# Kernel optimization log

Hardware: AMD Instinct MI355X
Metric: run time of the kernel (lower is better)

Reference implementation:

```python
import jax, jax.numpy as jnp
import numpy as np

DIM = 256
WINDOW = 512  # look_backward=1, look_forward=0, causal


def setup_inputs() -> dict:
    key = jax.random.key(0)
    ks = jax.random.split(key, 7)
    B, N, D = 8, 8192, DIM
    s = D ** -0.5
    return {
        "x": jax.random.normal(ks[0], (B, D, N), dtype=jnp.float32),
        "Wq": jax.random.normal(ks[1], (D, D), dtype=jnp.float32) * s,
        "bq": jax.random.normal(ks[2], (D,), dtype=jnp.float32) * 0.01,
        "Wk": jax.random.normal(ks[3], (D, D), dtype=jnp.float32) * s,
        "bk": jax.random.normal(ks[4], (D,), dtype=jnp.float32) * 0.01,
        "Wv": jax.random.normal(ks[5], (D, D), dtype=jnp.float32) * s,
        "bv": jax.random.normal(ks[6], (D,), dtype=jnp.float32) * 0.01,
    }


def _local_attention(q, k, v, window):
    # q,k,v: (B, N, D); causal sliding-window attention, look_backward=1 window.
    b, n, d = q.shape
    nw = n // window  # N assumed multiple of window (autopad no-op here)
    scale = d ** -0.5
    qb = q.reshape(b, nw, window, d)
    kb = k.reshape(b, nw, window, d)
    vb = v.reshape(b, nw, window, d)

    def look_back(t):
        prev = jnp.pad(t, ((0, 0), (1, 0), (0, 0), (0, 0)))[:, :-1]
        return jnp.concatenate([prev, t], axis=2)  # (b, nw, 2*window, d)

    kb2 = look_back(kb)
    vb2 = look_back(vb)

    pos = jnp.arange(n).reshape(nw, window)
    prev_pos = jnp.pad(pos, ((1, 0), (0, 0)), constant_values=-1)[:-1]
    kpos = jnp.concatenate([prev_pos, pos], axis=1)  # (nw, 2*window)
    # causal mask + mask out the (nonexistent) window before window 0
    mask = (pos[:, :, None] >= kpos[:, None, :]) & (kpos[:, None, :] >= 0)

    scores = jnp.einsum('bnqd,bnkd->bnqk', qb, kb2) * scale
    scores = jnp.where(mask[None], scores, jnp.asarray(-1e9, scores.dtype))
    attn = jax.nn.softmax(scores, axis=-1)  # dropout(0.1) omitted: eval mode
    out = jnp.einsum('bnqk,bnkd->bnqd', attn, vb2)
    return out.reshape(b, n, d)


def reference(x, Wq, bq, Wk, bk, Wv, bv):
    # x: (B, D, N) -> permute -> (B, N, D)
    xp = jnp.transpose(x, (0, 2, 1))
    q = xp @ Wq.T + bq
    k = xp @ Wk.T + bk
    v = xp @ Wv.T + bv
    y = xp + _local_attention(q, k, v, WINDOW)  # residual
    return jnp.transpose(y, (0, 2, 1))
```

## Files before the change

kernel.cpp:

```cpp
#include <hip/hip_runtime.h>
#include <hip/hip_bf16.h>

#define DIM  256
#define NSEQ 8192
#define BATCH 8
#define WIN  512

typedef __attribute__((ext_vector_type(8))) short short8;
typedef __attribute__((ext_vector_type(4))) float floatx4;

union PFU { int i[4]; short8 v; };

__device__ __forceinline__ int packbf(float a, float b) {
    __hip_bfloat162 h;
    h.x = __float2bfloat16(a);
    h.y = __float2bfloat16(b);
    int r;
    __builtin_memcpy(&r, &h, 4);
    return r;
}

__global__ __launch_bounds__(256) void k_wcast(const float* __restrict__ w0,
                                               const float* __restrict__ w1,
                                               const float* __restrict__ w2,
                                               __hip_bfloat16* __restrict__ wb) {
    int i = (blockIdx.x * 256 + threadIdx.x) * 4;
    const float* s = (i < 65536) ? (w0 + i) : ((i < 131072) ? (w1 + i - 65536) : (w2 + i - 131072));
    float4 v = *(const float4*)s;
    union { __hip_bfloat16 h[4]; ushort4 u; } cv;
    cv.h[0] = __float2bfloat16(v.x);
    cv.h[1] = __float2bfloat16(v.y);
    cv.h[2] = __float2bfloat16(v.z);
    cv.h[3] = __float2bfloat16(v.w);
    *(ushort4*)(wb + i) = cv.u;
}

__global__ __launch_bounds__(256, 3) void k_prep(const float* __restrict__ x,
                                                 const __hip_bfloat16* __restrict__ wb,
                                                 const float* __restrict__ bq,
                                                 const float* __restrict__ bk,
                                                 const float* __restrict__ bv,
                                                 __hip_bfloat16* __restrict__ qo,
                                                 __hip_bfloat16* __restrict__ ko,
                                                 __hip_bfloat16* __restrict__ vto) {
    __shared__ float ftile[64][68];
    __shared__ __align__(16) char As[32768];
    const int b   = blockIdx.y;
    const int n0  = blockIdx.x * 64;
    const int tid = threadIdx.x;
    const int wv  = tid >> 6;
    const int l   = tid & 63;
    const int lm  = l & 15;
    const int qd  = l >> 4;
    const int wn  = wv * 64;

    const float* xb = x + (size_t)b * DIM * NSEQ;

    const int dr = l >> 4, nseg = l & 15;
#pragma unroll
    for (int dsl = 0; dsl < 4; ++dsl) {
        const int d0 = dsl * 64;
#pragma unroll
        for (int i = 0; i < 4; ++i) {
            const int r = wv * 16 + i * 4 + dr;
            float4 v = *(const float4*)(xb + (size_t)(d0 + r) * NSEQ + n0 + nseg * 4);
            *(float4*)&ftile[r][nseg * 4] = v;
        }
        __syncthreads();
#pragma unroll
        for (int p = 0; p < 2; ++p) {
            const int ks = dsl * 2 + p;
            int4 pk;
            int* pki = (int*)&pk;
#pragma unroll
            for (int jj = 0; jj < 4; ++jj)
                pki[jj] = packbf(ftile[p * 32 + wv * 8 + jj * 2][l],
                                 ftile[p * 32 + wv * 8 + jj * 2 + 1][l]);
            *(int4*)(As + ks * 4096 + wv * 1024 + l * 16) = pk;
        }
        __syncthreads();
    }

#pragma unroll
    for (int mode = 0; mode < 3; ++mode) {
        const __hip_bfloat16* wp = wb + mode * 65536;
        floatx4 acc[4][4];
#pragma unroll
        for (int i = 0; i < 4; ++i)
#pragma unroll
            for (int j = 0; j < 4; ++j) acc[i][j] = (floatx4){0.f, 0.f, 0.f, 0.f};

#pragma unroll
        for (int ks = 0; ks < 8; ++ks) {
            short8 wf[4], af[4];
#pragma unroll
            for (int j = 0; j < 4; ++j)
                wf[j] = *(const short8*)(wp + (size_t)(wn + j * 16 + lm) * DIM + ks * 32 + qd * 8);
#pragma unroll
            for (int j = 0; j < 4; ++j)
                af[j] = *(const short8*)(As + ks * 4096 + qd * 1024 + (j * 16 + lm) * 16);
            if (mode < 2) {
#pragma unroll
                for (int mt = 0; mt < 4; ++mt)
#pragma unroll
                    for (int nt = 0; nt < 4; ++nt)
                        acc[mt][nt] = __builtin_amdgcn_mfma_f32_16x16x32_bf16(af[mt], wf[nt], acc[mt][nt], 0, 0, 0);
            } else {
#pragma unroll
                for (int jw = 0; jw < 4; ++jw)
#pragma unroll
                    for (int ja = 0; ja < 4; ++ja)
                        acc[jw][ja] = __builtin_amdgcn_mfma_f32_16x16x32_bf16(wf[jw], af[ja], acc[jw][ja], 0, 0, 0);
            }
        }

        if (mode < 2) {
            const float* bias = mode ? bk : bq;
            __hip_bfloat16* op = (mode ? ko : qo) + (size_t)b * NSEQ * DIM;
            float bc[4];
#pragma unroll
            for (int nt = 0; nt < 4; ++nt) bc[nt] = bias[wn + nt * 16 + lm];
#pragma unroll
            for (int mt = 0; mt < 4; ++mt)
#pragma unroll
                for (int nt = 0; nt < 4; ++nt)
#pragma unroll
                    for (int r = 0; r < 4; ++r)
                        op[(size_t)(n0 + mt * 16 + qd * 4 + r) * DIM + wn + nt * 16 + lm] =
                            __float2bfloat16(acc[mt][nt][r] + bc[nt]);
        } else {
            __hip_bfloat16* op = vto + (size_t)b * DIM * NSEQ;
#pragma unroll
            for (int jw = 0; jw < 4; ++jw)
#pragma unroll
                for (int r = 0; r < 4; ++r) {
                    const int d = wn + jw * 16 + qd * 4 + r;
                    const float bb = bv[d];
#pragma unroll
                    for (int ja = 0; ja < 4; ++ja)
                        op[(size_t)d * NSEQ + n0 + ja * 16 + lm] =
                            __float2bfloat16(acc[jw][ja][r] + bb);
                }
        }
    }
}

__global__ __launch_bounds__(512, 2) void k_attn(const __hip_bfloat16* __restrict__ qm,
                                                 const __hip_bfloat16* __restrict__ km,
                                                 const __hip_bfloat16* __restrict__ vtm,
                                                 const float* __restrict__ x,
                                                 float* __restrict__ out) {
    __shared__ __align__(16) char kbuf[2][16384];
    __shared__ __align__(16) char vbuf[2][16384];

    const int w  = blockIdx.x, b = blockIdx.y, qt = blockIdx.z;
    const int tid = threadIdx.x;
    const int wv = tid >> 6;
    const int l  = tid & 63;
    const int m  = l & 15;
    const int qd = l >> 4;

    const int qbw   = qt * 256 + wv * 32;
    const int koff0 = w * WIN - WIN;

    short8 qf[2][8];
#pragma unroll
    for (int u = 0; u < 2; ++u) {
        const __hip_bfloat16* qrow =
            qm + ((size_t)b * NSEQ + (size_t)(w * WIN + qbw + u * 16 + m)) * DIM;
#pragma unroll
        for (int s = 0; s < 8; ++s)
            qf[u][s] = *(const short8*)(qrow + s * 32 + qd * 8);
    }

    const char* kbase = (const char*)(km + (size_t)b * NSEQ * DIM);
    const char* vbase = (const char*)(vtm + (size_t)b * DIM * NSEQ);

    const int c0  = (w == 0) ? 16 : 0;
    const int c1w = (512 + qbw + 63) >> 5;
    const int c1b = (799 + qt * 256) >> 5;

    const bool   isK     = wv < 4;
    const size_t gstride = isK ? (size_t)64 : (size_t)16 * NSEQ * 2;
    const size_t adv     = isK ? (size_t)32 * 512 : (size_t)64;
    const int    lbase   = (isK ? wv * 4 : (wv - 4) * 4) * 1024 + l * 16;
    const char* gp0;
    if (isK)
        gp0 = kbase + (size_t)(koff0 + c0 * 32 + (wv >> 1) * 16 + m) * 512 +
              (size_t)((wv & 1) * 16 + qd) * 16;
    else
        gp0 = vbase + (size_t)((wv - 4) * 64 + m) * (NSEQ * 2) +
              (size_t)(koff0 + c0 * 32) * 2 + (size_t)qd * 16;

    floatx4 o[2][16];
#pragma unroll
    for (int u = 0; u < 2; ++u)
#pragma unroll
        for (int t = 0; t < 16; ++t) o[u][t] = (floatx4){0.f, 0.f, 0.f, 0.f};
    float mi[2] = {-INFINITY, -INFINITY};
    float li[2] = {0.f, 0.f};
    const float sscale = 0.0625f * 1.4426950408889634f;

    const int a0 = (((qd & 1) * 2) * 16 + m) * 4;
    const int a1 = a0 + 64;
    const bool hi = (qd >> 1) != 0;

    int4 rg[4];
#pragma unroll
    for (int i = 0; i < 4; ++i)
        rg[i] = *(const int4*)(gp0 + (size_t)i * gstride);
    gp0 += adv;
    {
        char* d0 = (isK ? kbuf[0] : vbuf[0]) + lbase;
#pragma unroll
        for (int i = 0; i < 4; ++i)
            *(int4*)(d0 + i * 1024) = rg[i];
    }
    __syncthreads();

    int pb = 0;
    for (int c = c0; c < c1b; ++c) {
        const bool more = (c + 1 < c1b);
        if (more) {
#pragma unroll
            for (int i = 0; i < 4; ++i)
                rg[i] = *(const int4*)(gp0 + (size_t)i * gstride);
            gp0 += adv;
        }
        if (c < c1w) {
            const char* kbp = kbuf[pb];
            floatx4 st[2][2];
#pragma unroll
            for (int u = 0; u < 2; ++u)
#pragma unroll
                for (int t = 0; t < 2; ++t) st[u][t] = (floatx4){0.f, 0.f, 0.f, 0.f};
            __builtin_amdgcn_s_setprio(1);
#pragma unroll
            for (int t = 0; t < 2; ++t)
#pragma unroll
                for (int s = 0; s < 8; ++s) {
                    short8 kf = *(const short8*)(kbp + ((t * 8 + s) * 64 + l) * 16);
                    st[0][t] = __builtin_amdgcn_mfma_f32_16x16x32_bf16(kf, qf[0][s], st[0][t], 0, 0, 0);
                    st[1][t] = __builtin_amdgcn_mfma_f32_16x16x32_bf16(kf, qf[1][s], st[1][t], 0, 0, 0);
                }
            __builtin_amdgcn_s_setprio(0);
            const int kl0 = c * 32;
            short8 pf[2];
#pragma unroll
            for (int u = 0; u < 2; ++u) {
                const int lim = 512 + qbw + u * 16 + m;
                const bool needmask = (kl0 + 31) > lim;
                float p[8];
#pragma unroll
                for (int t = 0; t < 2; ++t)
#pragma unroll
                    for (int r = 0; r < 4; ++r) {
                        float v = st[u][t][r] * sscale;
                        if (needmask) {
                            int key = kl0 + t * 16 + qd * 4 + r;
                            v = (key <= lim) ? v : -INFINITY;
                        }
                        p[t * 4 + r] = v;
                    }
                float mx = p[0];
#pragma unroll
                for (int i = 1; i < 8; ++i) mx = fmaxf(mx, p[i]);
                mx = fmaxf(mx, __shfl_xor(mx, 16, 64));
                mx = fmaxf(mx, __shfl_xor(mx, 32, 64));
                float mnew;
                if (__all(mx <= mi[u] + 8.0f)) mnew = mi[u];
                else                           mnew = fmaxf(mi[u], mx);
                const float alpha = exp2f(mi[u] - mnew);
                float ps = 0.f;
#pragma unroll
                for (int i = 0; i < 8; ++i) { p[i] = exp2f(p[i] - mnew); ps += p[i]; }
                ps += __shfl_xor(ps, 16, 64);
                ps += __shfl_xor(ps, 32, 64);
                li[u] = li[u] * alpha + ps;
                mi[u] = mnew;
                if (!__all(alpha == 1.0f)) {
#pragma unroll
                    for (int t = 0; t < 16; ++t) {
                        o[u][t][0] *= alpha; o[u][t][1] *= alpha;
                        o[u][t][2] *= alpha; o[u][t][3] *= alpha;
                    }
                }
                int pd0 = packbf(p[0], p[1]);
                int pd1 = packbf(p[2], p[3]);
                int pd2 = packbf(p[4], p[5]);
                int pd3 = packbf(p[6], p[7]);
                int x0 = __builtin_amdgcn_ds_bpermute(a0, pd0);
                int y0 = __builtin_amdgcn_ds_bpermute(a0, pd2);
                int x1 = __builtin_amdgcn_ds_bpermute(a0, pd1);
                int y1 = __builtin_amdgcn_ds_bpermute(a0, pd3);
                int x2 = __builtin_amdgcn_ds_bpermute(a1, pd0);
                int y2 = __builtin_amdgcn_ds_bpermute(a1, pd2);
                int x3 = __builtin_amdgcn_ds_bpermute(a1, pd1);
                int y3 = __builtin_amdgcn_ds_bpermute(a1, pd3);
                PFU pu;
                pu.i[0] = hi ? y0 : x0;
                pu.i[1] = hi ? y1 : x1;
                pu.i[2] = hi ? y2 : x2;
                pu.i[3] = hi ? y3 : x3;
                pf[u] = pu.v;
            }
            const char* vbp = vbuf[pb];
            __builtin_amdgcn_s_setprio(1);
#pragma unroll
            for (int t = 0; t < 16; ++t) {
                short8 vf = *(const short8*)(vbp + (t * 64 + l) * 16);
                o[0][t] = __builtin_amdgcn_mfma_f32_16x16x32_bf16(vf, pf[0], o[0][t], 0, 0, 0);
                o[1][t] = __builtin_amdgcn_mfma_f32_16x16x32_bf16(vf, pf[1], o[1][t], 0, 0, 0);
            }
            __builtin_amdgcn_s_setprio(0);
        }
        if (more) {
            char* dst = (isK ? kbuf[pb ^ 1] : vbuf[pb ^ 1]) + lbase;
#pragma unroll
            for (int i = 0; i < 4; ++i)
                *(int4*)(dst + i * 1024) = rg[i];
        }
        __syncthreads();
        pb ^= 1;
    }

#pragma unroll
    for (int u = 0; u < 2; ++u) {
        const float inv = 1.f / li[u];
        const int ng = w * WIN + qbw + u * 16 + m;
        const float* xr  = x   + (size_t)b * DIM * NSEQ + ng;
        float*       orw = out + (size_t)b * DIM * NSEQ + ng;
#pragma unroll
        for (int t = 0; t < 16; ++t)
#pragma unroll
            for (int r = 0; r < 4; ++r) {
                int d = t * 16 + qd * 4 + r;
                orw[(size_t)d * NSEQ] = xr[(size_t)d * NSEQ] + o[u][t][r] * inv;
            }
    }
}

extern "C" void kernel_launch(void* const* d_in, const int* in_sizes, int n_in,
                              void* d_out, int out_size, void* d_ws, size_t ws_size,
                              hipStream_t stream) {
    const float* x  = (const float*)d_in[0];
    const float* Wq = (const float*)d_in[1];
    const float* bq = (const float*)d_in[2];
    const float* Wk = (const float*)d_in[3];
    const float* bk = (const float*)d_in[4];
    const float* Wv = (const float*)d_in[5];
    const float* bv = (const float*)d_in[6];

    char* ws = (char*)d_ws;
    const size_t SZ = (size_t)BATCH * NSEQ * DIM * sizeof(__hip_bfloat16);
    __hip_bfloat16* qb_ = (__hip_bfloat16*)(ws);
    __hip_bfloat16* kb_ = (__hip_bfloat16*)(ws + SZ);
    __hip_bfloat16* vt_ = (__hip_bfloat16*)(ws + 2 * SZ);
    __hip_bfloat16* wb_ = (__hip_bfloat16*)(ws + 3 * SZ);

    k_wcast<<<dim3(192), 256, 0, stream>>>(Wq, Wk, Wv, wb_);
    k_prep<<<dim3(NSEQ / 64, BATCH), 256, 0, stream>>>(x, wb_, bq, bk, bv, qb_, kb_, vt_);
    k_attn<<<dim3(16, BATCH, 2), 512, 0, stream>>>(qb_, kb_, vt_, x, (float*)d_out);
}
```

Before: 347.6 us.

## Fuse weight cast into projection kernel and software-pipeline QK with triple buffering

Drops the separate weight-cast kernel: the projection kernel now reads fp32 weights and packs them to bf16 in registers, which saves one launch but doubles weight load bytes and adds conversion ALU in the inner loop. The attention kernel moves from two K/V shared-memory buffers to three and prefetches two chunks ahead. It also computes the next chunk's QK scores before the current chunk's softmax and PV, so the matrix-core work can overlap the softmax. The cost is more LDS per block (96KB) and more live registers, which may cut occupancy from two blocks per CU.

```diff
diff --git a/kernel.cpp b/kernel.cpp
--- a/kernel.cpp
+++ b/kernel.cpp
@@ -20,23 +20,10 @@
     return r;
 }
 
-__global__ __launch_bounds__(256) void k_wcast(const float* __restrict__ w0,
-                                               const float* __restrict__ w1,
-                                               const float* __restrict__ w2,
-                                               __hip_bfloat16* __restrict__ wb) {
-    int i = (blockIdx.x * 256 + threadIdx.x) * 4;
-    const float* s = (i < 65536) ? (w0 + i) : ((i < 131072) ? (w1 + i - 65536) : (w2 + i - 131072));
-    float4 v = *(const float4*)s;
-    union { __hip_bfloat16 h[4]; ushort4 u; } cv;
-    cv.h[0] = __float2bfloat16(v.x);
-    cv.h[1] = __float2bfloat16(v.y);
-    cv.h[2] = __float2bfloat16(v.z);
-    cv.h[3] = __float2bfloat16(v.w);
-    *(ushort4*)(wb + i) = cv.u;
-}
-
 __global__ __launch_bounds__(256, 3) void k_prep(const float* __restrict__ x,
-                                                 const __hip_bfloat16* __restrict__ wb,
+                                                 const float* __restrict__ Wq,
+                                                 const float* __restrict__ Wk,
+                                                 const float* __restrict__ Wv,
                                                  const float* __restrict__ bq,
                                                  const float* __restrict__ bk,
                                                  const float* __restrict__ bv,
@@ -83,7 +70,7 @@
 
 #pragma unroll
     for (int mode = 0; mode < 3; ++mode) {
-        const __hip_bfloat16* wp = wb + mode * 65536;
+        const float* wsrc = (mode == 0) ? Wq : ((mode == 1) ? Wk : Wv);
         floatx4 acc[4][4];
 #pragma unroll
         for (int i = 0; i < 4; ++i)
@@ -94,8 +81,17 @@
         for (int ks = 0; ks < 8; ++ks) {
             short8 wf[4], af[4];
 #pragma unroll
-            for (int j = 0; j < 4; ++j)
-                wf[j] = *(const short8*)(wp + (size_t)(wn + j * 16 + lm) * DIM + ks * 32 + qd * 8);
+            for (int j = 0; j < 4; ++j) {
+                const float* wr = wsrc + (size_t)(wn + j * 16 + lm) * 256 + ks * 32 + qd * 8;
+                float4 wa = *(const float4*)wr;
+                float4 wc = *(const float4*)(wr + 4);
+                PFU pw;
+                pw.i[0] = packbf(wa.x, wa.y);
+                pw.i[1] = packbf(wa.z, wa.w);
+                pw.i[2] = packbf(wc.x, wc.y);
+                pw.i[3] = packbf(wc.z, wc.w);
+                wf[j] = pw.v;
+            }
 #pragma unroll
             for (int j = 0; j < 4; ++j)
                 af[j] = *(const short8*)(As + ks * 4096 + qd * 1024 + (j * 16 + lm) * 16);
@@ -150,8 +146,8 @@
                                                  const __hip_bfloat16* __restrict__ vtm,
                                                  const float* __restrict__ x,
                                                  float* __restrict__ out) {
-    __shared__ __align__(16) char kbuf[2][16384];
-    __shared__ __align__(16) char vbuf[2][16384];
+    __shared__ __align__(16) char kbuf[3][16384];
+    __shared__ __align__(16) char vbuf[3][16384];
 
     const int w  = blockIdx.x, b = blockIdx.y, qt = blockIdx.z;
     const int tid = threadIdx.x;
@@ -205,6 +201,23 @@
     const int a1 = a0 + 64;
     const bool hi = (qd >> 1) != 0;
 
+    auto QK = [&](const char* kbp, floatx4 (&stt)[2][2]) {
+#pragma unroll
+        for (int u = 0; u < 2; ++u)
+#pragma unroll
+            for (int t = 0; t < 2; ++t) stt[u][t] = (floatx4){0.f, 0.f, 0.f, 0.f};
+        __builtin_amdgcn_s_setprio(1);
+#pragma unroll
+        for (int t = 0; t < 2; ++t)
+#pragma unroll
+            for (int s = 0; s < 8; ++s) {
+                short8 kf = *(const short8*)(kbp + ((t * 8 + s) * 64 + l) * 16);
+                stt[0][t] = __builtin_amdgcn_mfma_f32_16x16x32_bf16(kf, qf[0][s], stt[0][t], 0, 0, 0);
+                stt[1][t] = __builtin_amdgcn_mfma_f32_16x16x32_bf16(kf, qf[1][s], stt[1][t], 0, 0, 0);
+            }
+        __builtin_amdgcn_s_setprio(0);
+    };
+
     int4 rg[4];
 #pragma unroll
     for (int i = 0; i < 4; ++i)
@@ -216,34 +229,34 @@
         for (int i = 0; i < 4; ++i)
             *(int4*)(d0 + i * 1024) = rg[i];
     }
+#pragma unroll
+    for (int i = 0; i < 4; ++i)
+        rg[i] = *(const int4*)(gp0 + (size_t)i * gstride);
+    gp0 += adv;
+    {
+        char* d1 = (isK ? kbuf[1] : vbuf[1]) + lbase;
+#pragma unroll
+        for (int i = 0; i < 4; ++i)
+            *(int4*)(d1 + i * 1024) = rg[i];
+    }
     __syncthreads();
 
-    int pb = 0;
+    floatx4 stc[2][2], stn[2][2];
+    QK(kbuf[0], stc);
+
+    int cur = 0, nxt = 1, fut = 2;
     for (int c = c0; c < c1b; ++c) {
-        const bool more = (c + 1 < c1b);
-        if (more) {
+        const bool more2 = (c + 2 < c1b);
+        if (more2) {
 #pragma unroll
             for (int i = 0; i < 4; ++i)
                 rg[i] = *(const int4*)(gp0 + (size_t)i * gstride);
             gp0 += adv;
         }
         if (c < c1w) {
-            const char* kbp = kbuf[pb];
-            floatx4 st[2][2];
-#pragma unroll
-            for (int u = 0; u < 2; ++u)
-#pragma unroll
-                for (int t = 0; t < 2; ++t) st[u][t] = (floatx4){0.f, 0.f, 0.f, 0.f};
-            __builtin_amdgcn_s_setprio(1);
-#pragma unroll
-            for (int t = 0; t < 2; ++t)
-#pragma unroll
-                for (int s = 0; s < 8; ++s) {
-                    short8 kf = *(const short8*)(kbp + ((t * 8 + s) * 64 + l) * 16);
-                    st[0][t] = __builtin_amdgcn_mfma_f32_16x16x32_bf16(kf, qf[0][s], st[0][t], 0, 0, 0);
-                    st[1][t] = __builtin_amdgcn_mfma_f32_16x16x32_bf16(kf, qf[1][s], st[1][t], 0, 0, 0);
-                }
-            __builtin_amdgcn_s_setprio(0);
+            const bool nn = (c + 1 < c1w);
+            if (nn) QK(kbuf[nxt], stn);
+
             const int kl0 = c * 32;
             short8 pf[2];
 #pragma unroll
@@ -255,7 +268,7 @@
                 for (int t = 0; t < 2; ++t)
 #pragma unroll
                     for (int r = 0; r < 4; ++r) {
-                        float v = st[u][t][r] * sscale;
+                        float v = stc[u][t][r] * sscale;
                         if (needmask) {
                             int key = kl0 + t * 16 + qd * 4 + r;
                             v = (key <= lim) ? v : -INFINITY;
@@ -304,7 +317,7 @@
                 pu.i[3] = hi ? y3 : x3;
                 pf[u] = pu.v;
             }
-            const char* vbp = vbuf[pb];
+            const char* vbp = vbuf[cur];
             __builtin_amdgcn_s_setprio(1);
 #pragma unroll
             for (int t = 0; t < 16; ++t) {
@@ -313,15 +326,21 @@
                 o[1][t] = __builtin_amdgcn_mfma_f32_16x16x32_bf16(vf, pf[1], o[1][t], 0, 0, 0);
             }
             __builtin_amdgcn_s_setprio(0);
-        }
-        if (more) {
-            char* dst = (isK ? kbuf[pb ^ 1] : vbuf[pb ^ 1]) + lbase;
+            if (nn) {
+#pragma unroll
+                for (int u = 0; u < 2; ++u)
+#pragma unroll
+                    for (int t = 0; t < 2; ++t) stc[u][t] = stn[u][t];
+            }
+        }
+        if (more2) {
+            char* dst = (isK ? kbuf[fut] : vbuf[fut]) + lbase;
 #pragma unroll
             for (int i = 0; i < 4; ++i)
                 *(int4*)(dst + i * 1024) = rg[i];
         }
         __syncthreads();
-        pb ^= 1;
+        const int t0 = cur; cur = nxt; nxt = fut; fut = t0;
     }
 
 #pragma unroll
@@ -356,9 +375,7 @@
     __hip_bfloat16* qb_ = (__hip_bfloat16*)(ws);
     __hip_bfloat16* kb_ = (__hip_bfloat16*)(ws + SZ);
     __hip_bfloat16* vt_ = (__hip_bfloat16*)(ws + 2 * SZ);
-    __hip_bfloat16* wb_ = (__hip_bfloat16*)(ws + 3 * SZ);
-
-    k_wcast<<<dim3(192), 256, 0, stream>>>(Wq, Wk, Wv, wb_);
-    k_prep<<<dim3(NSEQ / 64, BATCH), 256, 0, stream>>>(x, wb_, bq, bk, bv, qb_, kb_, vt_);
+
+    k_prep<<<dim3(NSEQ / 64, BATCH), 256, 0, stream>>>(x, Wq, Wk, Wv, bq, bk, bv, qb_, kb_, vt_);
     k_attn<<<dim3(16, BATCH, 2), 512, 0, stream>>>(qb_, kb_, vt_, x, (float*)d_out);
 }
```

Result: slower. 453.7 us (+30.5%).

## Use 16 waves per attention block with one 16-row query tile each

Applied to the files above, without the earlier changes.

The attention block grows from 8 to 16 wavefronts (1024 threads). Each wave now owns one 16-row query tile instead of two, so per-wave registers (Q fragments, output accumulators, softmax state) are halved and the K/V tile loads are spread over twice as many waves. The aim is more waves in flight to hide latency and less register pressure. In exchange, each K/V fragment read from LDS feeds only one MFMA instead of two, so LDS traffic per unit of work doubles and barrier cost rises with more waves per block.

```diff
diff --git a/kernel.cpp b/kernel.cpp
--- a/kernel.cpp
+++ b/kernel.cpp
@@ -145,11 +145,11 @@
     }
 }
 
-__global__ __launch_bounds__(512, 2) void k_attn(const __hip_bfloat16* __restrict__ qm,
-                                                 const __hip_bfloat16* __restrict__ km,
-                                                 const __hip_bfloat16* __restrict__ vtm,
-                                                 const float* __restrict__ x,
-                                                 float* __restrict__ out) {
+__global__ __launch_bounds__(1024, 4) void k_attn(const __hip_bfloat16* __restrict__ qm,
+                                                  const __hip_bfloat16* __restrict__ km,
+                                                  const __hip_bfloat16* __restrict__ vtm,
+                                                  const float* __restrict__ x,
+                                                  float* __restrict__ out) {
     __shared__ __align__(16) char kbuf[2][16384];
     __shared__ __align__(16) char vbuf[2][16384];
 
@@ -160,60 +160,58 @@
     const int m  = l & 15;
     const int qd = l >> 4;
 
-    const int qbw   = qt * 256 + wv * 32;
+    const int qbw   = qt * 256 + wv * 16;
     const int koff0 = w * WIN - WIN;
 
-    short8 qf[2][8];
-#pragma unroll
-    for (int u = 0; u < 2; ++u) {
+    short8 qf[8];
+    {
         const __hip_bfloat16* qrow =
-            qm + ((size_t)b * NSEQ + (size_t)(w * WIN + qbw + u * 16 + m)) * DIM;
+            qm + ((size_t)b * NSEQ + (size_t)(w * WIN + qbw + m)) * DIM;
 #pragma unroll
         for (int s = 0; s < 8; ++s)
-            qf[u][s] = *(const short8*)(qrow + s * 32 + qd * 8);
+            qf[s] = *(const short8*)(qrow + s * 32 + qd * 8);
     }
 
     const char* kbase = (const char*)(km + (size_t)b * NSEQ * DIM);
     const char* vbase = (const char*)(vtm + (size_t)b * DIM * NSEQ);
 
     const int c0  = (w == 0) ? 16 : 0;
-    const int c1w = (512 + qbw + 63) >> 5;
+    const int c1w = (512 + qbw + 47) >> 5;
     const int c1b = (799 + qt * 256) >> 5;
 
-    const bool   isK     = wv < 4;
+    const bool   isK = wv < 8;
+    const int    wk  = wv & 7;
     const size_t gstride = isK ? (size_t)64 : (size_t)16 * NSEQ * 2;
     const size_t adv     = isK ? (size_t)32 * 512 : (size_t)64;
-    const int    lbase   = (isK ? wv * 4 : (wv - 4) * 4) * 1024 + l * 16;
+    const int    lbase   = wk * 2048 + l * 16;
     const char* gp0;
     if (isK)
-        gp0 = kbase + (size_t)(koff0 + c0 * 32 + (wv >> 1) * 16 + m) * 512 +
-              (size_t)((wv & 1) * 16 + qd) * 16;
+        gp0 = kbase + (size_t)(koff0 + c0 * 32 + (wk >> 2) * 16 + m) * 512 +
+              (size_t)(((wk >> 1) & 1) * 16 + qd) * 16 + (size_t)(wk & 1) * 128;
     else
-        gp0 = vbase + (size_t)((wv - 4) * 64 + m) * (NSEQ * 2) +
+        gp0 = vbase + (size_t)((wk >> 1) * 64 + (wk & 1) * 32 + m) * (NSEQ * 2) +
               (size_t)(koff0 + c0 * 32) * 2 + (size_t)qd * 16;
 
-    floatx4 o[2][16];
-#pragma unroll
-    for (int u = 0; u < 2; ++u)
-#pragma unroll
-        for (int t = 0; t < 16; ++t) o[u][t] = (floatx4){0.f, 0.f, 0.f, 0.f};
-    float mi[2] = {-INFINITY, -INFINITY};
-    float li[2] = {0.f, 0.f};
+    floatx4 o[16];
+#pragma unroll
+    for (int t = 0; t < 16; ++t) o[t] = (floatx4){0.f, 0.f, 0.f, 0.f};
+    float mi = -INFINITY;
+    float li = 0.f;
     const float sscale = 0.0625f * 1.4426950408889634f;
 
     const int a0 = (((qd & 1) * 2) * 16 + m) * 4;
     const int a1 = a0 + 64;
     const bool hi = (qd >> 1) != 0;
 
-    int4 rg[4];
-#pragma unroll
-    for (int i = 0; i < 4; ++i)
+    int4 rg[2];
+#pragma unroll
+    for (int i = 0; i < 2; ++i)
         rg[i] = *(const int4*)(gp0 + (size_t)i * gstride);
     gp0 += adv;
     {
         char* d0 = (isK ? kbuf[0] : vbuf[0]) + lbase;
 #pragma unroll
-        for (int i = 0; i < 4; ++i)
+        for (int i = 0; i < 2; ++i)
             *(int4*)(d0 + i * 1024) = rg[i];
     }
     __syncthreads();
@@ -223,111 +221,102 @@
         const bool more = (c + 1 < c1b);
         if (more) {
 #pragma unroll
-            for (int i = 0; i < 4; ++i)
+            for (int i = 0; i < 2; ++i)
                 rg[i] = *(const int4*)(gp0 + (size_t)i * gstride);
             gp0 += adv;
         }
         if (c < c1w) {
             const char* kbp = kbuf[pb];
-            floatx4 st[2][2];
-#pragma unroll
-            for (int u = 0; u < 2; ++u)
-#pragma unroll
-                for (int t = 0; t < 2; ++t) st[u][t] = (floatx4){0.f, 0.f, 0.f, 0.f};
+            floatx4 st[2];
+            st[0] = (floatx4){0.f, 0.f, 0.f, 0.f};
+            st[1] = (floatx4){0.f, 0.f, 0.f, 0.f};
             __builtin_amdgcn_s_setprio(1);
 #pragma unroll
             for (int t = 0; t < 2; ++t)
 #pragma unroll
                 for (int s = 0; s < 8; ++s) {
                     short8 kf = *(const short8*)(kbp + ((t * 8 + s) * 64 + l) * 16);
-                    st[0][t] = __builtin_amdgcn_mfma_f32_16x16x32_bf16(kf, qf[0][s], st[0][t], 0, 0, 0);
-                    st[1][t] = __builtin_amdgcn_mfma_f32_16x16x32_bf16(kf, qf[1][s], st[1][t], 0, 0, 0);
+                    st[t] = __builtin_amdgcn_mfma_f32_16x16x32_bf16(kf, qf[s], st[t], 0, 0, 0);
                 }
             __builtin_amdgcn_s_setprio(0);
             const int kl0 = c * 32;
-            short8 pf[2];
-#pragma unroll
-            for (int u = 0; u < 2; ++u) {
-                const int lim = 512 + qbw + u * 16 + m;
-                const bool needmask = (kl0 + 31) > lim;
-                float p[8];
-#pragma unroll
-                for (int t = 0; t < 2; ++t)
-#pragma unroll
-                    for (int r = 0; r < 4; ++r) {
-                        float v = st[u][t][r] * sscale;
-                        if (needmask) {
-                            int key = kl0 + t * 16 + qd * 4 + r;
-                            v = (key <= lim) ? v : -INFINITY;
-                        }
-                        p[t * 4 + r] = v;
+            const int lim = 512 + qbw + m;
+            const bool needmask = (kl0 + 31) > lim;
+            float p[8];
+#pragma unroll
+            for (int t = 0; t < 2; ++t)
+#pragma unroll
+                for (int r = 0; r < 4; ++r) {
+                    float v = st[t][r] * sscale;
+                    if (needmask) {
+                        int key = kl0 + t * 16 + qd * 4 + r;
+                        v = (key <= lim) ? v : -INFINITY;
                     }
-                float mx = p[0];
-#pragma unroll
-                for (int i = 1; i < 8; ++i) mx = fmaxf(mx, p[i]);
-                mx = fmaxf(mx, __shfl_xor(mx, 16, 64));
-                mx = fmaxf(mx, __shfl_xor(mx, 32, 64));
-                float mnew;
-                if (__all(mx <= mi[u] + 8.0f)) mnew = mi[u];
-                else                           mnew = fmaxf(mi[u], mx);
-                const float alpha = exp2f(mi[u] - mnew);
-                float ps = 0.f;
-#pragma unroll
-                for (int i = 0; i < 8; ++i) { p[i] = exp2f(p[i] - mnew); ps += p[i]; }
-                ps += __shfl_xor(ps, 16, 64);
-                ps += __shfl_xor(ps, 32, 64);
-                li[u] = li[u] * alpha + ps;
-                mi[u] = mnew;
-                if (!__all(alpha == 1.0f)) {
-#pragma unroll
-                    for (int t = 0; t < 16; ++t) {
-                        o[u][t][0] *= alpha; o[u][t][1] *= alpha;
-                        o[u][t][2] *= alpha; o[u][t][3] *= alpha;
-                    }
+                    p[t * 4 + r] = v;
                 }
-                int pd0 = packbf(p[0], p[1]);
-                int pd1 = packbf(p[2], p[3]);
-                int pd2 = packbf(p[4], p[5]);
-                int pd3 = packbf(p[6], p[7]);
-                int x0 = __builtin_amdgcn_ds_bpermute(a0, pd0);
-                int y0 = __builtin_amdgcn_ds_bpermute(a0, pd2);
-                int x1 = __builtin_amdgcn_ds_bpermute(a0, pd1);
-                int y1 = __builtin_amdgcn_ds_bpermute(a0, pd3);
-                int x2 = __builtin_amdgcn_ds_bpermute(a1, pd0);
-                int y2 = __builtin_amdgcn_ds_bpermute(a1, pd2);
-                int x3 = __builtin_amdgcn_ds_bpermute(a1, pd1);
-                int y3 = __builtin_amdgcn_ds_bpermute(a1, pd3);
-                PFU pu;
-                pu.i[0] = hi ? y0 : x0;
-                pu.i[1] = hi ? y1 : x1;
-                pu.i[2] = hi ? y2 : x2;
-                pu.i[3] = hi ? y3 : x3;
-                pf[u] = pu.v;
+            float mx = p[0];
+#pragma unroll
+            for (int i = 1; i < 8; ++i) mx = fmaxf(mx, p[i]);
+            mx = fmaxf(mx, __shfl_xor(mx, 16, 64));
+            mx = fmaxf(mx, __shfl_xor(mx, 32, 64));
+            float mnew;
+            if (__all(mx <= mi + 8.0f)) mnew = mi;
+            else                        mnew = fmaxf(mi, mx);
+            const float alpha = exp2f(mi - mnew);
+            float ps = 0.f;
+#pragma unroll
+            for (int i = 0; i < 8; ++i) { p[i] = exp2f(p[i] - mnew); ps += p[i]; }
+            ps += __shfl_xor(ps, 16, 64);
+            ps += __shfl_xor(ps, 32, 64);
+            li = li * alpha + ps;
+            mi = mnew;
+            if (!__all(alpha == 1.0f)) {
+#pragma unroll
+                for (int t = 0; t < 16; ++t) {
+                    o[t][0] *= alpha; o[t][1] *= alpha;
+                    o[t][2] *= alpha; o[t][3] *= alpha;
+                }
             }
+            int pd0 = packbf(p[0], p[1]);
+            int pd1 = packbf(p[2], p[3]);
+            int pd2 = packbf(p[4], p[5]);
+            int pd3 = packbf(p[6], p[7]);
+            int x0 = __builtin_amdgcn_ds_bpermute(a0, pd0);
+            int y0 = __builtin_amdgcn_ds_bpermute(a0, pd2);
+            int x1 = __builtin_amdgcn_ds_bpermute(a0, pd1);
+            int y1 = __builtin_amdgcn_ds_bpermute(a0, pd3);
+            int x2 = __builtin_amdgcn_ds_bpermute(a1, pd0);
+            int y2 = __builtin_amdgcn_ds_bpermute(a1, pd2);
+            int x3 = __builtin_amdgcn_ds_bpermute(a1, pd1);
+            int y3 = __builtin_amdgcn_ds_bpermute(a1, pd3);
+            PFU pu;
+            pu.i[0] = hi ? y0 : x0;
+            pu.i[1] = hi ? y1 : x1;
+            pu.i[2] = hi ? y2 : x2;
+            pu.i[3] = hi ? y3 : x3;
+            short8 pf = pu.v;
             const char* vbp = vbuf[pb];
             __builtin_amdgcn_s_setprio(1);
 #pragma unroll
             for (int t = 0; t < 16; ++t) {
                 short8 vf = *(const short8*)(vbp + (t * 64 + l) * 16);
-                o[0][t] = __builtin_amdgcn_mfma_f32_16x16x32_bf16(vf, pf[0], o[0][t], 0, 0, 0);
-                o[1][t] = __builtin_amdgcn_mfma_f32_16x16x32_bf16(vf, pf[1], o[1][t], 0, 0, 0);
+                o[t] = __builtin_amdgcn_mfma_f32_16x16x32_bf16(vf, pf, o[t], 0, 0, 0);
             }
             __builtin_amdgcn_s_setprio(0);
         }
         if (more) {
             char* dst = (isK ? kbuf[pb ^ 1] : vbuf[pb ^ 1]) + lbase;
 #pragma unroll
-            for (int i = 0; i < 4; ++i)
+            for (int i = 0; i < 2; ++i)
                 *(int4*)(dst + i * 1024) = rg[i];
         }
         __syncthreads();
         pb ^= 1;
     }
 
-#pragma unroll
-    for (int u = 0; u < 2; ++u) {
-        const float inv = 1.f / li[u];
-        const int ng = w * WIN + qbw + u * 16 + m;
+    {
+        const float inv = 1.f / li;
+        const int ng = w * WIN + qbw + m;
         const float* xr  = x   + (size_t)b * DIM * NSEQ + ng;
         float*       orw = out + (size_t)b * DIM * NSEQ + ng;
 #pragma unroll
@@ -335,7 +324,7 @@
 #pragma unroll
             for (int r = 0; r < 4; ++r) {
                 int d = t * 16 + qd * 4 + r;
-                orw[(size_t)d * NSEQ] = xr[(size_t)d * NSEQ] + o[u][t][r] * inv;
+                orw[(size_t)d * NSEQ] = xr[(size_t)d * NSEQ] + o[t][r] * inv;
             }
     }
 }
@@ -360,5 +349,5 @@
 
     k_wcast<<<dim3(192), 256, 0, stream>>>(Wq, Wk, Wv, wb_);
     k_prep<<<dim3(NSEQ / 64, BATCH), 256, 0, stream>>>(x, wb_, bq, bk, bv, qb_, kb_, vt_);
-    k_attn<<<dim3(16, BATCH, 2), 512, 0, stream>>>(qb_, kb_, vt_, x, (float*)d_out);
-}
+    k_attn<<<dim3(16, BATCH, 2), 1024, 0, stream>>>(qb_, kb_, vt_, x, (float*)d_out);
+}
```

Result: faster. 336.1 us (-3.3%).
